# Performance work log

Measured on AMD Instinct MI355X. Metric: run time of the kernel, lower is better.

The kernel has to match this reference:

```python
import jax, jax.numpy as jnp
import numpy as np

DILATION = 1
THETA = 1.0
K = 3 + 2 * (DILATION - 1)  # 3x3 window


def setup_inputs() -> dict:
    key = jax.random.key(0)
    x = jax.random.normal(key, (8, 64, 224, 224), dtype=jnp.float32)
    return {"x": x}


def _extract_patches(x, k, d):
    # x: [b, c, h, w] -> patches: [b, c, k*k, h, w], zero-padded like F.unfold(padding=d)
    b, c, h, w = x.shape
    xp = jnp.pad(x, ((0, 0), (0, 0), (d, d), (d, d)))
    return jnp.stack(
        [xp[:, :, i * d:i * d + h, j * d:j * d + w] for i in range(k) for j in range(k)],
        axis=2,
    )


def reference(x) -> jnp.ndarray:
    b, c, h, w = x.shape
    patches = _extract_patches(x, K, DILATION)  # [b, c, kk, h, w]

    mean = patches.mean(axis=2, keepdims=True)
    # torch .std() is unbiased (ddof=1)
    std = jnp.clip(jnp.std(patches, axis=2, keepdims=True, ddof=1), 1e-3, None)
    normed = (patches - mean) / std

    contrast = (normed ** 2).mean(axis=2)
    energy = (patches ** 2).mean(axis=2)
    clamped = jnp.clip(patches, 1e-6, None)
    entropy = -(clamped * jnp.log(clamped)).mean(axis=2)
    homogeneity = 1.0 / ((1.0 + jnp.abs(patches - mean)).mean(axis=2) + 1e-6)

    feats = jnp.stack([contrast, energy, entropy, homogeneity], axis=2)  # [b, c, 4, h, w]

    log_feat = jnp.log(jnp.clip(feats, 1e-5, None))
    martingale = jnp.clip(jnp.exp(THETA * log_feat - 0.5 * THETA ** 2), 1e-4, 1e4)
    martingale = jnp.where(jnp.isfinite(martingale), martingale, jnp.ones_like(martingale))

    # per-channel feature stacks concatenated along channel dim -> [b, c*4, h, w]
    return martingale.reshape(b, c * 4, h, w)
```

## Files before the change

kernel.cpp:

```cpp
#include <hip/hip_runtime.h>
#include <math.h>

#define B 8
#define C 64
#define H 224
#define W 224
#define HW (H * W)
#define TW 32
#define TH 32
#define HS 2

typedef float v4f __attribute__((ext_vector_type(4)));

__global__ __launch_bounds__(128, 8) void medseg_kernel(const float* __restrict__ x,
                                                        float* __restrict__ out) {
    const int plane = blockIdx.z;
    const int w0 = blockIdx.x * TW;
    const int tid = threadIdx.x;
    const int tx = tid & 7;
    const int g  = tid >> 3;
    const int cb = w0 + 4 * tx;
    const int h0 = blockIdx.y * TH + g * HS;

    const float* __restrict__ xp = x + (size_t)plane * HW;
    const bool lb = (cb > 0);
    const bool rb = (cb + 4 < W);

    float win[3][6];

    auto loadrow = [&](int r, float w[6]) {
        const bool rin = (r >= 0) && (r < H);
        const float* rowp = xp + r * W;
        float4 bq = rin ? *(const float4*)(rowp + cb) : make_float4(0.f, 0.f, 0.f, 0.f);
        float al = (rin && lb) ? rowp[cb - 1] : 0.0f;
        float cr = (rin && rb) ? rowp[cb + 4] : 0.0f;
        w[0] = al; w[1] = bq.x; w[2] = bq.y; w[3] = bq.z; w[4] = bq.w; w[5] = cr;
    };

    loadrow(h0 - 1, win[0]);
    loadrow(h0,     win[1]);
    loadrow(h0 + 1, win[2]);

    const float EXPM  = 0.6065306597126334f;
    const float E9    = EXPM / 9.0f;
    const float NL9   = -0.6931471805599453f * EXPM / 9.0f;
    const float CONTR = 0.5391383641890075f;

    float* ob0 = out + ((size_t)plane * 4) * HW + (size_t)h0 * W + cb;

    #pragma unroll
    for (int it = 0; it < HS; ++it) {
        const int s0 = it % 3, s1 = (it + 1) % 3, s2 = (it + 2) % 3;

        float pre[6];
        if (it < HS - 1) loadrow(h0 + it + 2, pre);

        float cs[6], cq[6], ce[6];
        #pragma unroll
        for (int j = 0; j < 6; ++j) {
            const float v0 = win[s0][j], v1 = win[s1][j], v2 = win[s2][j];
            cs[j] = v0 + v1 + v2;
            cq[j] = fmaf(v0, v0, fmaf(v1, v1, v2 * v2));
            const float c0 = fmaxf(v0, 1e-6f), c1 = fmaxf(v1, 1e-6f), c2 = fmaxf(v2, 1e-6f);
            ce[j] = fmaf(c0, __log2f(c0), fmaf(c1, __log2f(c1), c2 * __log2f(c2)));
        }

        float oe[4], ot[4], oh[4];
        #pragma unroll
        for (int k = 0; k < 4; ++k) {
            const float s1v = cs[k] + cs[k + 1] + cs[k + 2];
            const float s2v = cq[k] + cq[k + 1] + cq[k + 2];
            const float sev = ce[k] + ce[k + 1] + ce[k + 2];
            const float mean = s1v * (1.0f / 9.0f);

            float sad = 0.0f;
            #pragma unroll
            for (int j = 0; j < 3; ++j) sad += fabsf(win[s0][k + j] - mean);
            #pragma unroll
            for (int j = 0; j < 3; ++j) sad += fabsf(win[s1][k + j] - mean);
            #pragma unroll
            for (int j = 0; j < 3; ++j) sad += fabsf(win[s2][k + j] - mean);

            oe[k] = fmaxf(s2v * E9, 1e-4f);
            ot[k] = fmaxf(sev * NL9, 1e-4f);
            const float denom = fmaf(sad, 1.0f / 9.0f, 1.000001f);
            oh[k] = fmaxf(EXPM * __builtin_amdgcn_rcpf(denom), 1e-4f);
        }

        float* ob = ob0 + (size_t)it * W;
        v4f vc = {CONTR, CONTR, CONTR, CONTR};
        v4f ve = {oe[0], oe[1], oe[2], oe[3]};
        v4f vt = {ot[0], ot[1], ot[2], ot[3]};
        v4f vh = {oh[0], oh[1], oh[2], oh[3]};
        *(v4f*)(ob + 0 * HW) = vc;
        *(v4f*)(ob + 1 * HW) = ve;
        *(v4f*)(ob + 2 * HW) = vt;
        *(v4f*)(ob + 3 * HW) = vh;

        if (it < HS - 1) {
            #pragma unroll
            for (int j = 0; j < 6; ++j) win[s0][j] = pre[j];
        }
    }
}

extern "C" void kernel_launch(void* const* d_in, const int* in_sizes, int n_in,
                              void* d_out, int out_size, void* d_ws, size_t ws_size,
                              hipStream_t stream) {
    const float* x = (const float*)d_in[0];
    float* out = (float*)d_out;
    dim3 grid(W / TW, H / TH, B * C);
    dim3 block(128);
    medseg_kernel<<<grid, block, 0, stream>>>(x, out);
}
```

Measured before the change: 531.3 us.

## Load all window rows upfront with branchless clamped loads and nontemporal stores

Each thread now computes four output rows instead of two, with 64-thread blocks, and loads its whole six-row window at the start. Out-of-range rows and columns are handled by clamping the addresses and multiplying by a 0/1 mask instead of branching. Output stores become nontemporal to avoid polluting the cache with write-only data. Together these aim to expose more memory parallelism per thread and cut branch overhead, at the cost of more registers and fewer threads per block.

```diff
diff --git a/kernel.cpp b/kernel.cpp
--- a/kernel.cpp
+++ b/kernel.cpp
@@ -8,12 +8,12 @@
 #define HW (H * W)
 #define TW 32
 #define TH 32
-#define HS 2
+#define HS 4
 
 typedef float v4f __attribute__((ext_vector_type(4)));
 
-__global__ __launch_bounds__(128, 8) void medseg_kernel(const float* __restrict__ x,
-                                                        float* __restrict__ out) {
+__global__ __launch_bounds__(64, 4) void medseg_kernel(const float* __restrict__ x,
+                                                       float* __restrict__ out) {
     const int plane = blockIdx.z;
     const int w0 = blockIdx.x * TW;
     const int tid = threadIdx.x;
@@ -23,23 +23,29 @@
     const int h0 = blockIdx.y * TH + g * HS;
 
     const float* __restrict__ xp = x + (size_t)plane * HW;
-    const bool lb = (cb > 0);
-    const bool rb = (cb + 4 < W);
 
-    float win[3][6];
+    const float ml = (cb > 0) ? 1.0f : 0.0f;
+    const float mr = (cb + 4 < W) ? 1.0f : 0.0f;
+    const int li = (cb > 0) ? cb - 1 : 0;
+    const int ri = (cb + 4 < W) ? cb + 4 : W - 1;
 
-    auto loadrow = [&](int r, float w[6]) {
-        const bool rin = (r >= 0) && (r < H);
-        const float* rowp = xp + r * W;
-        float4 bq = rin ? *(const float4*)(rowp + cb) : make_float4(0.f, 0.f, 0.f, 0.f);
-        float al = (rin && lb) ? rowp[cb - 1] : 0.0f;
-        float cr = (rin && rb) ? rowp[cb + 4] : 0.0f;
-        w[0] = al; w[1] = bq.x; w[2] = bq.y; w[3] = bq.z; w[4] = bq.w; w[5] = cr;
-    };
-
-    loadrow(h0 - 1, win[0]);
-    loadrow(h0,     win[1]);
-    loadrow(h0 + 1, win[2]);
+    float win[6][6];
+    #pragma unroll
+    for (int r = 0; r < 6; ++r) {
+        const int row = h0 - 1 + r;
+        const int rc = (row < 0) ? 0 : ((row > H - 1) ? H - 1 : row);
+        const float* rowp = xp + rc * W;
+        const float4 bq = *(const float4*)(rowp + cb);
+        const float al = rowp[li];
+        const float cr = rowp[ri];
+        const float mrow = (row >= 0 && row < H) ? 1.0f : 0.0f;
+        win[r][0] = al * (ml * mrow);
+        win[r][1] = bq.x * mrow;
+        win[r][2] = bq.y * mrow;
+        win[r][3] = bq.z * mrow;
+        win[r][4] = bq.w * mrow;
+        win[r][5] = cr * (mr * mrow);
+    }
 
     const float EXPM  = 0.6065306597126334f;
     const float E9    = EXPM / 9.0f;
@@ -47,18 +53,14 @@
     const float CONTR = 0.5391383641890075f;
 
     float* ob0 = out + ((size_t)plane * 4) * HW + (size_t)h0 * W + cb;
+    const v4f vc = {CONTR, CONTR, CONTR, CONTR};
 
     #pragma unroll
     for (int it = 0; it < HS; ++it) {
-        const int s0 = it % 3, s1 = (it + 1) % 3, s2 = (it + 2) % 3;
-
-        float pre[6];
-        if (it < HS - 1) loadrow(h0 + it + 2, pre);
-
         float cs[6], cq[6], ce[6];
         #pragma unroll
         for (int j = 0; j < 6; ++j) {
-            const float v0 = win[s0][j], v1 = win[s1][j], v2 = win[s2][j];
+            const float v0 = win[it][j], v1 = win[it + 1][j], v2 = win[it + 2][j];
             cs[j] = v0 + v1 + v2;
             cq[j] = fmaf(v0, v0, fmaf(v1, v1, v2 * v2));
             const float c0 = fmaxf(v0, 1e-6f), c1 = fmaxf(v1, 1e-6f), c2 = fmaxf(v2, 1e-6f);
@@ -75,11 +77,10 @@
 
             float sad = 0.0f;
             #pragma unroll
-            for (int j = 0; j < 3; ++j) sad += fabsf(win[s0][k + j] - mean);
-            #pragma unroll
-            for (int j = 0; j < 3; ++j) sad += fabsf(win[s1][k + j] - mean);
-            #pragma unroll
-            for (int j = 0; j < 3; ++j) sad += fabsf(win[s2][k + j] - mean);
+            for (int d = 0; d < 3; ++d)
+                #pragma unroll
+                for (int j = 0; j < 3; ++j)
+                    sad += fabsf(win[it + d][k + j] - mean);
 
             oe[k] = fmaxf(s2v * E9, 1e-4f);
             ot[k] = fmaxf(sev * NL9, 1e-4f);
@@ -88,19 +89,13 @@
         }
 
         float* ob = ob0 + (size_t)it * W;
-        v4f vc = {CONTR, CONTR, CONTR, CONTR};
         v4f ve = {oe[0], oe[1], oe[2], oe[3]};
         v4f vt = {ot[0], ot[1], ot[2], ot[3]};
         v4f vh = {oh[0], oh[1], oh[2], oh[3]};
-        *(v4f*)(ob + 0 * HW) = vc;
-        *(v4f*)(ob + 1 * HW) = ve;
-        *(v4f*)(ob + 2 * HW) = vt;
-        *(v4f*)(ob + 3 * HW) = vh;
-
-        if (it < HS - 1) {
-            #pragma unroll
-            for (int j = 0; j < 6; ++j) win[s0][j] = pre[j];
-        }
+        __builtin_nontemporal_store(vc, (v4f*)(ob + 0 * HW));
+        __builtin_nontemporal_store(ve, (v4f*)(ob + 1 * HW));
+        __builtin_nontemporal_store(vt, (v4f*)(ob + 2 * HW));
+        __builtin_nontemporal_store(vh, (v4f*)(ob + 3 * HW));
     }
 }
 
@@ -110,6 +105,6 @@
     const float* x = (const float*)d_in[0];
     float* out = (float*)d_out;
     dim3 grid(W / TW, H / TH, B * C);
-    dim3 block(128);
+    dim3 block(64);
     medseg_kernel<<<grid, block, 0, stream>>>(x, out);
 }
```

New measurement: 482.5 us. 9.2% less time.
